# Kernel tuning notes

Hardware: AMD Instinct MI355X
Metric: run time of the kernel (lower is better)

The kernel has to match this reference:

```python
import jax, jax.numpy as jnp
import numpy as np

V, D, NL = 32000, 768, 4
DI, N, DC, DTR = 2 * D, 16, 4, 48  # d_inner, d_state, d_conv, dt_rank
B, L = 2, 1024


def _rmsnorm(x, w, eps=1e-5):
    var = jnp.mean(x * x, axis=-1, keepdims=True)
    return x * jax.lax.rsqrt(var + eps) * w


def _causal_depthwise_conv(x, w, b):
    # x: (B, L, DI), w: (DI, DC), b: (DI,)
    xc = x.transpose(0, 2, 1)  # (B, DI, L)
    out = jax.lax.conv_general_dilated(
        xc, w[:, None, :], window_strides=(1,), padding=[(DC - 1, 0)],
        dimension_numbers=("NCH", "OIH", "NCH"), feature_group_count=DI)
    return (out + b[None, :, None]).transpose(0, 2, 1)


def _selective_scan(u, delta, A, Bm, Cm, Dv):
    # u,delta: (B,L,DI); A: (DI,N); Bm,Cm: (B,L,N); Dv: (DI,)
    dA = jnp.exp(delta[..., None] * A)                       # (B,L,DI,N)
    dBu = delta[..., None] * Bm[:, :, None, :] * u[..., None]  # (B,L,DI,N)

    def step(h, inp):
        dA_t, dBu_t, C_t = inp
        h = dA_t * h + dBu_t                                  # (B,DI,N)
        y = jnp.einsum("bdn,bn->bd", h, C_t)
        return h, y

    h0 = jnp.zeros((u.shape[0], DI, N), u.dtype)
    _, ys = jax.lax.scan(step, h0, (dA.transpose(1, 0, 2, 3),
                                    dBu.transpose(1, 0, 2, 3),
                                    Cm.transpose(1, 0, 2)))
    return ys.transpose(1, 0, 2) + u * Dv


def _mamba_block(x, norm_w, in_w, conv_w, conv_b, xproj_w, dt_w, dt_b,
                 A_log, Dv, out_w):
    xn = _rmsnorm(x, norm_w)
    xz = jnp.einsum("bld,ed->ble", xn, in_w)                 # (B,L,2*DI)
    xb, z = jnp.split(xz, 2, axis=-1)
    xb = jax.nn.silu(_causal_depthwise_conv(xb, conv_w, conv_b))
    x_dbl = jnp.einsum("bld,ed->ble", xb, xproj_w)           # (B,L,DTR+2N)
    dt, Bm, Cm = jnp.split(x_dbl, [DTR, DTR + N], axis=-1)
    delta = jax.nn.softplus(jnp.einsum("blr,dr->bld", dt, dt_w) + dt_b)
    y = _selective_scan(xb, delta, -jnp.exp(A_log), Bm, Cm, Dv)
    y = y * jax.nn.silu(z)
    return x + jnp.einsum("ble,de->bld", y, out_w)


def setup_inputs() -> dict:
    key = jax.random.key(0)
    ks = jax.random.split(key, 16)
    s = lambda k, shape, sc=0.02: jax.random.normal(k, shape, jnp.float32) * sc
    dt_init = jnp.log(jnp.expm1(
        jnp.exp(jax.random.uniform(ks[12], (NL, DI), jnp.float32,
                                   np.log(1e-3), np.log(1e-1)))))
    return {
        "tokens": jax.random.randint(ks[0], (B, L), 0, V),
        "embedding": s(ks[1], (V, D)),
        "W_out_w": s(ks[2], (V, D)),
        "W_out_b": jnp.zeros((V,), jnp.float32),
        "norm_w": jnp.ones((NL, D), jnp.float32),
        "in_proj_w": s(ks[3], (NL, 2 * DI, D)),
        "conv_w": s(ks[4], (NL, DI, DC), 0.1),
        "conv_b": jnp.zeros((NL, DI), jnp.float32),
        "x_proj_w": s(ks[5], (NL, DTR + 2 * N, DI)),
        "dt_proj_w": s(ks[6], (NL, DI, DTR), 0.1),
        "dt_proj_b": dt_init,
        "A_log": jnp.log(jnp.broadcast_to(
            jnp.arange(1, N + 1, dtype=jnp.float32), (NL, DI, N))),
        "D": jnp.ones((NL, DI), jnp.float32),
        "out_proj_w": s(ks[7], (NL, D, DI)),
    }


def reference(tokens, embedding, W_out_w, W_out_b, norm_w, in_proj_w,
              conv_w, conv_b, x_proj_w, dt_proj_w, dt_proj_b, A_log, D,
              out_proj_w):
    x = embedding[tokens]                                    # (B,L,D)
    for i in range(NL):
        x = _mamba_block(x, norm_w[i], in_proj_w[i], conv_w[i], conv_b[i],
                         x_proj_w[i], dt_proj_w[i], dt_proj_b[i],
                         A_log[i], D[i], out_proj_w[i])
    return jnp.einsum("bld,vd->blv", x, W_out_w) + W_out_b
```

## Files before the change

### kernel.cpp

```cpp
#include <hip/hip_runtime.h>
#include <hip/hip_bf16.h>
#include <math.h>

#define BB   2
#define LL   1024
#define DD   768
#define DIN  1536
#define NS   16
#define DCV  4
#define DTRK 48
#define NLAY 4
#define VV   32000
#define ROWS (BB*LL)

#define NCH  32
#define CLEN (LL/NCH)

typedef __attribute__((ext_vector_type(8))) short short8;
typedef __attribute__((ext_vector_type(4))) float f32x4;


__global__ __launch_bounds__(256) void embed_kernel(
    const int* __restrict__ tok, const float* __restrict__ emb,
    float* __restrict__ x) {
  int idx = blockIdx.x * 256 + threadIdx.x;
  int row = idx / DD, c = idx - row * DD;
  x[idx] = emb[(size_t)tok[row] * DD + c];
}

__device__ __forceinline__ void cvt4_bf16(const float* __restrict__ in,
                                          __hip_bfloat16* __restrict__ out,
                                          int i) {
  float4 v = ((const float4*)in)[i];
  __hip_bfloat16 t0 = __float2bfloat16(v.x);
  __hip_bfloat16 t1 = __float2bfloat16(v.y);
  __hip_bfloat16 t2 = __float2bfloat16(v.z);
  __hip_bfloat16 t3 = __float2bfloat16(v.w);
  ushort4 pack = make_ushort4(*(unsigned short*)&t0, *(unsigned short*)&t1,
                              *(unsigned short*)&t2, *(unsigned short*)&t3);
  ((ushort4*)out)[i] = pack;
}

__global__ __launch_bounds__(256) void cvt_bf16_kernel(
    const float* __restrict__ in, __hip_bfloat16* __restrict__ out, int n4) {
  int i = blockIdx.x * 256 + threadIdx.x;
  if (i >= n4) return;
  cvt4_bf16(in, out, i);
}

__global__ __launch_bounds__(256) void cvt3_bf16_kernel(
    const float* __restrict__ i0, __hip_bfloat16* __restrict__ o0, int n0,
    const float* __restrict__ i1, __hip_bfloat16* __restrict__ o1, int n1,
    const float* __restrict__ i2, __hip_bfloat16* __restrict__ o2, int n2) {
  int start = blockIdx.x * 256 + threadIdx.x;
  int stride = gridDim.x * 256;
  for (int j = start; j < n0; j += stride) cvt4_bf16(i0, o0, j);
  for (int j = start; j < n1; j += stride) cvt4_bf16(i1, o1, j);
  for (int j = start; j < n2; j += stride) cvt4_bf16(i2, o2, j);
}

__global__ __launch_bounds__(256) void zero_kernel(float* __restrict__ p,
                                                   int n) {
  int i = blockIdx.x * 256 + threadIdx.x;
  if (i < n) p[i] = 0.0f;
}

__global__ __launch_bounds__(256) void rmsnorm_kernel(
    const float* __restrict__ x, const float* __restrict__ w,
    __hip_bfloat16* __restrict__ xn) {
  int row = blockIdx.x;
  int t = threadIdx.x;
  const float* xr = x + (size_t)row * DD;
  float v0 = xr[t], v1 = xr[t + 256], v2 = xr[t + 512];
  float ss = v0 * v0 + v1 * v1 + v2 * v2;
#pragma unroll
  for (int off = 32; off > 0; off >>= 1) ss += __shfl_down(ss, off);
  __shared__ float sred[4];
  if ((t & 63) == 0) sred[t >> 6] = ss;
  __syncthreads();
  float tot = sred[0] + sred[1] + sred[2] + sred[3];
  float scale = rsqrtf(tot * (1.0f / DD) + 1e-5f);
  __hip_bfloat16* xo = xn + (size_t)row * DD;
  xo[t]       = __float2bfloat16(v0 * scale * w[t]);
  xo[t + 256] = __float2bfloat16(v1 * scale * w[t + 256]);
  xo[t + 512] = __float2bfloat16(v2 * scale * w[t + 512]);
}

__global__ __launch_bounds__(256) void conv_silu_kernel(
    const float* __restrict__ xz, const float* __restrict__ cw,
    const float* __restrict__ cb, float* __restrict__ xb) {
  int idx = blockIdx.x * 256 + threadIdx.x;
  int row = idx / (DIN / 4);
  int d4 = idx - row * (DIN / 4);
  int d = d4 << 2;
  int l = row & (LL - 1);
  const float* col = xz + (size_t)row * (2 * DIN) + d;
  float4 x0 = *(const float4*)col;
  float4 x1 = make_float4(0, 0, 0, 0), x2 = x1, x3 = x1;
  if (l >= 1) x1 = *(const float4*)(col - 2 * DIN);
  if (l >= 2) x2 = *(const float4*)(col - 4 * DIN);
  if (l >= 3) x3 = *(const float4*)(col - 6 * DIN);
  float4 bb = *(const float4*)(cb + d);
  float4 wa = *(const float4*)(cw + (size_t)(d + 0) * 4);
  float4 wb = *(const float4*)(cw + (size_t)(d + 1) * 4);
  float4 wc = *(const float4*)(cw + (size_t)(d + 2) * 4);
  float4 wd = *(const float4*)(cw + (size_t)(d + 3) * 4);
  float4 r;
  r.x = bb.x + wa.w * x0.x + wa.z * x1.x + wa.y * x2.x + wa.x * x3.x;
  r.y = bb.y + wb.w * x0.y + wb.z * x1.y + wb.y * x2.y + wb.x * x3.y;
  r.z = bb.z + wc.w * x0.z + wc.z * x1.z + wc.y * x2.z + wc.x * x3.z;
  r.w = bb.w + wd.w * x0.w + wd.z * x1.w + wd.y * x2.w + wd.x * x3.w;
  r.x = r.x / (1.0f + __expf(-r.x));
  r.y = r.y / (1.0f + __expf(-r.y));
  r.z = r.z / (1.0f + __expf(-r.z));
  r.w = r.w / (1.0f + __expf(-r.w));
  *(float4*)(xb + (size_t)row * DIN + d) = r;
}

__device__ __forceinline__ float softplus_f(float t) {
  return t > 20.0f ? t : log1pf(__expf(t));
}

template <int EPI>
__global__ __launch_bounds__(256) void sgemm_nt(
    const float* __restrict__ A, int lda,
    const float* __restrict__ W, int ldw,
    float* __restrict__ C, int ldc,
    int N, int K, const float* __restrict__ bias) {
  __shared__ float As[16][68];
  __shared__ float Ws[16][68];
  const int tid = threadIdx.x;
  const int tx = tid & 15, ty = tid >> 4;
  const int bm = blockIdx.x, bn = blockIdx.y;
  const int kLen = K / gridDim.z;
  const int kBegin = blockIdx.z * kLen;
  const int kEnd = kBegin + kLen;
  const int lrow = tid >> 2;
  const int lk4 = (tid & 3) << 2;
  const float* Aptr = A + (size_t)(bm * 64 + lrow) * lda + lk4;
  const int wrow = bn * 64 + lrow;
  const float* Wptr = W + (size_t)wrow * ldw + lk4;
  const bool wvalid = wrow < N;
  float c[4][4] = {};
  for (int k0 = kBegin; k0 < kEnd; k0 += 16) {
    float4 a4 = *(const float4*)(Aptr + k0);
    float4 w4 = wvalid ? *(const float4*)(Wptr + k0) : make_float4(0, 0, 0, 0);
    __syncthreads();
    As[lk4 + 0][lrow] = a4.x; As[lk4 + 1][lrow] = a4.y;
    As[lk4 + 2][lrow] = a4.z; As[lk4 + 3][lrow] = a4.w;
    Ws[lk4 + 0][lrow] = w4.x; Ws[lk4 + 1][lrow] = w4.y;
    Ws[lk4 + 2][lrow] = w4.z; Ws[lk4 + 3][lrow] = w4.w;
    __syncthreads();
#pragma unroll
    for (int k = 0; k < 16; k++) {
      float4 a = *(const float4*)&As[k][ty << 2];
      float4 w = *(const float4*)&Ws[k][tx << 2];
      c[0][0] += a.x * w.x; c[0][1] += a.x * w.y; c[0][2] += a.x * w.z; c[0][3] += a.x * w.w;
      c[1][0] += a.y * w.x; c[1][1] += a.y * w.y; c[1][2] += a.y * w.z; c[1][3] += a.y * w.w;
      c[2][0] += a.z * w.x; c[2][1] += a.z * w.y; c[2][2] += a.z * w.z; c[2][3] += a.z * w.w;
      c[3][0] += a.w * w.x; c[3][1] += a.w * w.y; c[3][2] += a.w * w.z; c[3][3] += a.w * w.w;
    }
  }
  const int m0 = bm * 64 + (ty << 2);
  const int n0 = bn * 64 + (tx << 2);
  const bool split = gridDim.z > 1;
#pragma unroll
  for (int i = 0; i < 4; i++) {
    float* crow = C + (size_t)(m0 + i) * ldc;
#pragma unroll
    for (int j = 0; j < 4; j++) {
      int n = n0 + j;
      if (n < N) {
        float v = c[i][j];
        if constexpr (EPI == 1) v = softplus_f(v + bias[n]);
        if (split) atomicAdd(&crow[n], v);
        else crow[n] = v;
      }
    }
  }
}


__device__ __forceinline__ void gload16(const void* g, void* l) {
  __builtin_amdgcn_global_load_lds(
      (const __attribute__((address_space(1))) void*)g,
      (__attribute__((address_space(3))) void*)l, 16, 0, 0);
}

template <int EPI>
__global__ __launch_bounds__(256) void bgemm_nt(
    const __hip_bfloat16* __restrict__ A, int lda,
    const __hip_bfloat16* __restrict__ W, int ldw,
    float* __restrict__ C, int ldc,
    int K, const float* __restrict__ bias) {
  __shared__ short As[2][128 * 32];
  __shared__ short Ws[2][128 * 32];
  const int tid = threadIdx.x;
  const int wave = tid >> 6, lane = tid & 63;
  const int wm = wave >> 1, wn = wave & 1;

  const int nbx = gridDim.x;
  const int nwg = nbx * gridDim.y;
  int flat = blockIdx.y * nbx + blockIdx.x;
  if ((nwg & 7) == 0) {
    int chunk = nwg >> 3;
    flat = (flat & 7) * chunk + (flat >> 3);
  }
  const int tileM = (flat % nbx) * 128, tileN = (flat / nbx) * 128;

  const short* Ag = (const short*)A;
  const short* Wg = (const short*)W;
  const int cid0 = tid, cid1 = tid + 256;
  const size_t aOff0 = (size_t)(tileM + (cid0 >> 2)) * lda + (cid0 & 3) * 8;
  const size_t aOff1 = (size_t)(tileM + (cid1 >> 2)) * lda + (cid1 & 3) * 8;
  const size_t wOff0 = (size_t)(tileN + (cid0 >> 2)) * ldw + (cid0 & 3) * 8;
  const size_t wOff1 = (size_t)(tileN + (cid1 >> 2)) * ldw + (cid1 & 3) * 8;
  const int wb0 = wave * 512, wb1 = 2048 + wave * 512;

  const int fr = lane & 15, fq = lane >> 4;
  f32x4 acc[4][4] = {};

  for (int k0 = 0; k0 < K; k0 += 64) {
    gload16(Ag + aOff0 + k0, As[0] + wb0);
    gload16(Ag + aOff1 + k0, As[0] + wb1);
    gload16(Wg + wOff0 + k0, Ws[0] + wb0);
    gload16(Wg + wOff1 + k0, Ws[0] + wb1);
    gload16(Ag + aOff0 + k0 + 32, As[1] + wb0);
    gload16(Ag + aOff1 + k0 + 32, As[1] + wb1);
    gload16(Wg + wOff0 + k0 + 32, Ws[1] + wb0);
    gload16(Wg + wOff1 + k0 + 32, Ws[1] + wb1);
    __syncthreads();
#pragma unroll
    for (int s = 0; s < 2; s++) {
      short8 afr[4], bfr[4];
#pragma unroll
      for (int t = 0; t < 4; t++) {
        afr[t] = *(const short8*)(As[s] + (wm * 64 + t * 16 + fr) * 32 + fq * 8);
        bfr[t] = *(const short8*)(Ws[s] + (wn * 64 + t * 16 + fr) * 32 + fq * 8);
      }
#pragma unroll
      for (int mt = 0; mt < 4; mt++)
#pragma unroll
        for (int nt = 0; nt < 4; nt++)
          acc[mt][nt] = __builtin_amdgcn_mfma_f32_16x16x32_bf16(
              afr[mt], bfr[nt], acc[mt][nt], 0, 0, 0);
    }
    __syncthreads();
  }

#pragma unroll
  for (int mt = 0; mt < 4; mt++) {
#pragma unroll
    for (int r = 0; r < 4; r++) {
      int row = tileM + wm * 64 + mt * 16 + fq * 4 + r;
      float* crow = C + (size_t)row * ldc;
#pragma unroll
      for (int nt = 0; nt < 4; nt++) {
        int col = tileN + wn * 64 + nt * 16 + fr;
        float v = acc[mt][nt][r];
        if constexpr (EPI == 2) v += crow[col];
        else if constexpr (EPI == 3) v += bias[col];
        crow[col] = v;
      }
    }
  }
}


__global__ __launch_bounds__(256) void scan_pass1(
    const float* __restrict__ u,
    const float* __restrict__ dlt,
    const float* __restrict__ xdbl,
    const float* __restrict__ A_log,
    float* __restrict__ qbuf,
    float* __restrict__ sdel) {
  const int d = blockIdx.x * 256 + threadIdx.x;
  const int c = blockIdx.y;
  const int b = blockIdx.z;
  float Ac2[NS];
  {
    const float* ar = A_log + (size_t)d * NS;
#pragma unroll
    for (int j = 0; j < NS; j++) Ac2[j] = -__expf(ar[j]) * 1.44269504f;
  }
  const int l0 = c * CLEN;
  const float* ur = u   + ((size_t)b * LL + l0) * DIN + d;
  const float* dr = dlt + ((size_t)b * LL + l0) * DIN + d;
  const float* br = xdbl + ((size_t)b * LL + l0) * 80 + DTRK;
  float h[NS];
#pragma unroll
  for (int j = 0; j < NS; j++) h[j] = 0.0f;
  float sd = 0.0f;
  for (int t = 0; t < CLEN; t++) {
    float dl = dr[(size_t)t * DIN];
    float ul = ur[(size_t)t * DIN];
    float Bv[NS];
    *(float4*)&Bv[0]  = *(const float4*)(br + (size_t)t * 80);
    *(float4*)&Bv[4]  = *(const float4*)(br + (size_t)t * 80 + 4);
    *(float4*)&Bv[8]  = *(const float4*)(br + (size_t)t * 80 + 8);
    *(float4*)&Bv[12] = *(const float4*)(br + (size_t)t * 80 + 12);
    sd += dl;
    float du = dl * ul;
#pragma unroll
    for (int j = 0; j < NS; j++)
      h[j] = exp2f(dl * Ac2[j]) * h[j] + du * Bv[j];
  }
  float* qo = qbuf + (((size_t)b * NCH + c) * DIN + d) * NS;
#pragma unroll
  for (int j = 0; j < NS; j += 4)
    *(float4*)(qo + j) = make_float4(h[j], h[j + 1], h[j + 2], h[j + 3]);
  sdel[((size_t)b * NCH + c) * DIN + d] = sd;
}

__global__ __launch_bounds__(256) void scan_pass2(
    const float* __restrict__ qbuf, const float* __restrict__ sdel,
    const float* __restrict__ A_log, float* __restrict__ hstart) {
  const int e = blockIdx.x * 256 + threadIdx.x;
  const int n = e & (NS - 1);
  const int d = e >> 4;
  const int b = blockIdx.y;
  float Ac2 = -__expf(A_log[(size_t)d * NS + n]) * 1.44269504f;
  float h = 0.0f;
  for (int c = 0; c < NCH; c++) {
    hstart[(((size_t)b * NCH + c) * DIN + d) * NS + n] = h;
    if (c + 1 < NCH) {
      float sd = sdel[((size_t)b * NCH + c) * DIN + d];
      float q  = qbuf[(((size_t)b * NCH + c) * DIN + d) * NS + n];
      h = exp2f(Ac2 * sd) * h + q;
    }
  }
}

__global__ __launch_bounds__(256) void scan_pass3(
    const float* __restrict__ u,
    const float* __restrict__ dlt,
    const float* __restrict__ xdbl,
    const float* __restrict__ xz,
    const float* __restrict__ A_log,
    const float* __restrict__ Dv,
    const float* __restrict__ hstart,
    __hip_bfloat16* __restrict__ y) {
  const int d = blockIdx.x * 256 + threadIdx.x;
  const int c = blockIdx.y;
  const int b = blockIdx.z;
  float Ac2[NS];
  {
    const float* ar = A_log + (size_t)d * NS;
#pragma unroll
    for (int j = 0; j < NS; j++) Ac2[j] = -__expf(ar[j]) * 1.44269504f;
  }
  const float Dd = Dv[d];
  float h[NS];
  {
    const float* hs = hstart + (((size_t)b * NCH + c) * DIN + d) * NS;
#pragma unroll
    for (int j = 0; j < NS; j += 4) {
      float4 hv = *(const float4*)(hs + j);
      h[j] = hv.x; h[j + 1] = hv.y; h[j + 2] = hv.z; h[j + 3] = hv.w;
    }
  }
  const int l0 = c * CLEN;
  const float* ur = u   + ((size_t)b * LL + l0) * DIN + d;
  const float* dr = dlt + ((size_t)b * LL + l0) * DIN + d;
  const float* br = xdbl + ((size_t)b * LL + l0) * 80 + DTRK;
  const float* cr = br + NS;
  const float* zr = xz + ((size_t)b * LL + l0) * (2 * DIN) + DIN + d;
  __hip_bfloat16* yr = y + ((size_t)b * LL + l0) * DIN + d;
  for (int t = 0; t < CLEN; t++) {
    float dl = dr[(size_t)t * DIN];
    float ul = ur[(size_t)t * DIN];
    float zl = zr[(size_t)t * (2 * DIN)];
    float Bv[NS], Cv[NS];
    *(float4*)&Bv[0]  = *(const float4*)(br + (size_t)t * 80);
    *(float4*)&Bv[4]  = *(const float4*)(br + (size_t)t * 80 + 4);
    *(float4*)&Bv[8]  = *(const float4*)(br + (size_t)t * 80 + 8);
    *(float4*)&Bv[12] = *(const float4*)(br + (size_t)t * 80 + 12);
    *(float4*)&Cv[0]  = *(const float4*)(cr + (size_t)t * 80);
    *(float4*)&Cv[4]  = *(const float4*)(cr + (size_t)t * 80 + 4);
    *(float4*)&Cv[8]  = *(const float4*)(cr + (size_t)t * 80 + 8);
    *(float4*)&Cv[12] = *(const float4*)(cr + (size_t)t * 80 + 12);
    float du = dl * ul;
    float acc = 0.0f;
#pragma unroll
    for (int j = 0; j < NS; j++) {
      h[j] = exp2f(dl * Ac2[j]) * h[j] + du * Bv[j];
      acc += h[j] * Cv[j];
    }
    acc += ul * Dd;
    float sig = 1.0f / (1.0f + __expf(-zl));
    yr[(size_t)t * DIN] = __float2bfloat16(acc * (zl * sig));
  }
}


extern "C" void kernel_launch(void* const* d_in, const int* in_sizes, int n_in,
                              void* d_out, int out_size, void* d_ws,
                              size_t ws_size, hipStream_t stream) {
  const int*   tokens    = (const int*)d_in[0];
  const float* embedding = (const float*)d_in[1];
  const float* W_out_w   = (const float*)d_in[2];
  const float* W_out_b   = (const float*)d_in[3];
  const float* norm_w    = (const float*)d_in[4];
  const float* in_proj_w = (const float*)d_in[5];
  const float* conv_w    = (const float*)d_in[6];
  const float* conv_b    = (const float*)d_in[7];
  const float* x_proj_w  = (const float*)d_in[8];
  const float* dt_proj_w = (const float*)d_in[9];
  const float* dt_proj_b = (const float*)d_in[10];
  const float* A_log     = (const float*)d_in[11];
  const float* Dvec      = (const float*)d_in[12];
  const float* out_proj_w= (const float*)d_in[13];
  float* out = (float*)d_out;

  float* ws = (float*)d_ws;
  float* x    = ws;
  float* xz   = x + (size_t)ROWS * DD;
  float* xb   = xz + (size_t)ROWS * 2 * DIN;
  float* xdbl = xb + (size_t)ROWS * DIN;
  float* dlt  = xdbl + (size_t)ROWS * 80;
  __hip_bfloat16* bfbase = (__hip_bfloat16*)(dlt + (size_t)ROWS * DIN);
  __hip_bfloat16* xnb  = bfbase;
  __hip_bfloat16* ybb  = xnb + (size_t)ROWS * DD;
  __hip_bfloat16* xbf  = ybb + (size_t)ROWS * DIN;
  __hip_bfloat16* wInB = xbf + (size_t)ROWS * DD;
  __hip_bfloat16* wOpB = wInB + (size_t)NLAY * 2 * DIN * DD;
  __hip_bfloat16* wLgB = wOpB + (size_t)NLAY * DD * DIN;
  float* qbuf   = (float*)(wLgB + (size_t)VV * DD);
  float* sdel   = qbuf + (size_t)BB * NCH * DIN * NS;
  float* hstart = sdel + (size_t)BB * NCH * DIN;

  cvt3_bf16_kernel<<<2048, 256, 0, stream>>>(
      in_proj_w, wInB, NLAY * 2 * DIN * DD / 4,
      out_proj_w, wOpB, NLAY * DD * DIN / 4,
      W_out_w, wLgB, VV * DD / 4);

  embed_kernel<<<ROWS * DD / 256, 256, 0, stream>>>(tokens, embedding, x);

  for (int i = 0; i < NLAY; i++) {
    rmsnorm_kernel<<<ROWS, 256, 0, stream>>>(x, norm_w + (size_t)i * DD, xnb);
    bgemm_nt<0><<<dim3(16, 24), 256, 0, stream>>>(
        xnb, DD, wInB + (size_t)i * 2 * DIN * DD, DD, xz, 2 * DIN, DD,
        nullptr);
    conv_silu_kernel<<<ROWS * DIN / 4 / 256, 256, 0, stream>>>(
        xz, conv_w + (size_t)i * DIN * DCV, conv_b + (size_t)i * DIN, xb);
    zero_kernel<<<ROWS * 80 / 256, 256, 0, stream>>>(xdbl, ROWS * 80);
    sgemm_nt<0><<<dim3(32, 2, 8), 256, 0, stream>>>(
        xb, DIN, x_proj_w + (size_t)i * (DTRK + 2 * NS) * DIN, DIN, xdbl,
        DTRK + 2 * NS, DTRK + 2 * NS, DIN, nullptr);
    sgemm_nt<1><<<dim3(32, 24), 256, 0, stream>>>(
        xdbl, DTRK + 2 * NS, dt_proj_w + (size_t)i * DIN * DTRK, DTRK, dlt,
        DIN, DIN, DTRK, dt_proj_b + (size_t)i * DIN);
    const float* Ai = A_log + (size_t)i * DIN * NS;
    scan_pass1<<<dim3(DIN / 256, NCH - 1, BB), 256, 0, stream>>>(
        xb, dlt, xdbl, Ai, qbuf, sdel);
    scan_pass2<<<dim3(DIN * NS / 256, BB), 256, 0, stream>>>(
        qbuf, sdel, Ai, hstart);
    scan_pass3<<<dim3(DIN / 256, NCH, BB), 256, 0, stream>>>(
        xb, dlt, xdbl, xz, Ai, Dvec + (size_t)i * DIN, hstart, ybb);
    bgemm_nt<2><<<dim3(16, 6), 256, 0, stream>>>(
        ybb, DIN, wOpB + (size_t)i * DD * DIN, DIN, x, DD, DIN, nullptr);
  }

  {
    int n4 = ROWS * DD / 4;
    cvt_bf16_kernel<<<(n4 + 255) / 256, 256, 0, stream>>>(x, xbf, n4);
  }
  bgemm_nt<3><<<dim3(16, 250), 256, 0, stream>>>(
      xbf, DD, wLgB, DD, out, VV, DD, W_out_b);
}
```

Measured before the change: 1.349 ms.

## Shrink bf16 GEMM N-tile to 64 and add split-K for out_proj

The bf16 MFMA GEMM now uses 128x64 output tiles instead of 128x128, which doubles the grid for the in_proj and logits GEMMs. It also gains a split-K path over gridDim.z whose partial results are accumulated into C with atomicAdd. The out_proj GEMM uses that path (K split in two, 384 blocks) to fill more CUs, and the xdbl zeroing kernel is replaced by hipMemsetAsync. The aim is more parallelism on the small GEMMs; the costs are lower data reuse per tile, more memory traffic on the large logits GEMM, and non-deterministic float atomics.

```diff
diff --git a/kernel.cpp b/kernel.cpp
--- a/kernel.cpp
+++ b/kernel.cpp
@@ -57,12 +57,6 @@
   for (int j = start; j < n0; j += stride) cvt4_bf16(i0, o0, j);
   for (int j = start; j < n1; j += stride) cvt4_bf16(i1, o1, j);
   for (int j = start; j < n2; j += stride) cvt4_bf16(i2, o2, j);
-}
-
-__global__ __launch_bounds__(256) void zero_kernel(float* __restrict__ p,
-                                                   int n) {
-  int i = blockIdx.x * 256 + threadIdx.x;
-  if (i < n) p[i] = 0.0f;
 }
 
 __global__ __launch_bounds__(256) void rmsnorm_kernel(
@@ -194,7 +188,7 @@
     float* __restrict__ C, int ldc,
     int K, const float* __restrict__ bias) {
   __shared__ short As[2][128 * 32];
-  __shared__ short Ws[2][128 * 32];
+  __shared__ short Ws[2][64 * 32];
   const int tid = threadIdx.x;
   const int wave = tid >> 6, lane = tid & 63;
   const int wm = wave >> 1, wn = wave & 1;
@@ -206,7 +200,10 @@
     int chunk = nwg >> 3;
     flat = (flat & 7) * chunk + (flat >> 3);
   }
-  const int tileM = (flat % nbx) * 128, tileN = (flat / nbx) * 128;
+  const int tileM = (flat % nbx) * 128, tileN = (flat / nbx) * 64;
+
+  const int kLen = K / gridDim.z;
+  const int kBegin = blockIdx.z * kLen, kEnd = kBegin + kLen;
 
   const short* Ag = (const short*)A;
   const short* Wg = (const short*)W;
@@ -214,40 +211,39 @@
   const size_t aOff0 = (size_t)(tileM + (cid0 >> 2)) * lda + (cid0 & 3) * 8;
   const size_t aOff1 = (size_t)(tileM + (cid1 >> 2)) * lda + (cid1 & 3) * 8;
   const size_t wOff0 = (size_t)(tileN + (cid0 >> 2)) * ldw + (cid0 & 3) * 8;
-  const size_t wOff1 = (size_t)(tileN + (cid1 >> 2)) * ldw + (cid1 & 3) * 8;
-  const int wb0 = wave * 512, wb1 = 2048 + wave * 512;
+  const int wb = wave * 512;
 
   const int fr = lane & 15, fq = lane >> 4;
-  f32x4 acc[4][4] = {};
-
-  for (int k0 = 0; k0 < K; k0 += 64) {
-    gload16(Ag + aOff0 + k0, As[0] + wb0);
-    gload16(Ag + aOff1 + k0, As[0] + wb1);
-    gload16(Wg + wOff0 + k0, Ws[0] + wb0);
-    gload16(Wg + wOff1 + k0, Ws[0] + wb1);
-    gload16(Ag + aOff0 + k0 + 32, As[1] + wb0);
-    gload16(Ag + aOff1 + k0 + 32, As[1] + wb1);
-    gload16(Wg + wOff0 + k0 + 32, Ws[1] + wb0);
-    gload16(Wg + wOff1 + k0 + 32, Ws[1] + wb1);
+  f32x4 acc[4][2] = {};
+
+  for (int k0 = kBegin; k0 < kEnd; k0 += 64) {
+#pragma unroll
+    for (int s = 0; s < 2; s++) {
+      gload16(Ag + aOff0 + k0 + s * 32, As[s] + wb);
+      gload16(Ag + aOff1 + k0 + s * 32, As[s] + 2048 + wb);
+      gload16(Wg + wOff0 + k0 + s * 32, Ws[s] + wb);
+    }
     __syncthreads();
 #pragma unroll
     for (int s = 0; s < 2; s++) {
-      short8 afr[4], bfr[4];
-#pragma unroll
-      for (int t = 0; t < 4; t++) {
+      short8 afr[4], bfr[2];
+#pragma unroll
+      for (int t = 0; t < 4; t++)
         afr[t] = *(const short8*)(As[s] + (wm * 64 + t * 16 + fr) * 32 + fq * 8);
-        bfr[t] = *(const short8*)(Ws[s] + (wn * 64 + t * 16 + fr) * 32 + fq * 8);
-      }
+#pragma unroll
+      for (int t = 0; t < 2; t++)
+        bfr[t] = *(const short8*)(Ws[s] + (wn * 32 + t * 16 + fr) * 32 + fq * 8);
 #pragma unroll
       for (int mt = 0; mt < 4; mt++)
 #pragma unroll
-        for (int nt = 0; nt < 4; nt++)
+        for (int nt = 0; nt < 2; nt++)
           acc[mt][nt] = __builtin_amdgcn_mfma_f32_16x16x32_bf16(
               afr[mt], bfr[nt], acc[mt][nt], 0, 0, 0);
     }
     __syncthreads();
   }
 
+  const bool split = gridDim.z > 1;
 #pragma unroll
   for (int mt = 0; mt < 4; mt++) {
 #pragma unroll
@@ -255,12 +251,16 @@
       int row = tileM + wm * 64 + mt * 16 + fq * 4 + r;
       float* crow = C + (size_t)row * ldc;
 #pragma unroll
-      for (int nt = 0; nt < 4; nt++) {
-        int col = tileN + wn * 64 + nt * 16 + fr;
+      for (int nt = 0; nt < 2; nt++) {
+        int col = tileN + wn * 32 + nt * 16 + fr;
         float v = acc[mt][nt][r];
-        if constexpr (EPI == 2) v += crow[col];
-        else if constexpr (EPI == 3) v += bias[col];
-        crow[col] = v;
+        if (split) {
+          atomicAdd(&crow[col], v);
+        } else {
+          if constexpr (EPI == 2) v += crow[col];
+          else if constexpr (EPI == 3) v += bias[col];
+          crow[col] = v;
+        }
       }
     }
   }
@@ -438,12 +438,12 @@
 
   for (int i = 0; i < NLAY; i++) {
     rmsnorm_kernel<<<ROWS, 256, 0, stream>>>(x, norm_w + (size_t)i * DD, xnb);
-    bgemm_nt<0><<<dim3(16, 24), 256, 0, stream>>>(
+    bgemm_nt<0><<<dim3(16, 48), 256, 0, stream>>>(
         xnb, DD, wInB + (size_t)i * 2 * DIN * DD, DD, xz, 2 * DIN, DD,
         nullptr);
     conv_silu_kernel<<<ROWS * DIN / 4 / 256, 256, 0, stream>>>(
         xz, conv_w + (size_t)i * DIN * DCV, conv_b + (size_t)i * DIN, xb);
-    zero_kernel<<<ROWS * 80 / 256, 256, 0, stream>>>(xdbl, ROWS * 80);
+    hipMemsetAsync(xdbl, 0, (size_t)ROWS * 80 * sizeof(float), stream);
     sgemm_nt<0><<<dim3(32, 2, 8), 256, 0, stream>>>(
         xb, DIN, x_proj_w + (size_t)i * (DTRK + 2 * NS) * DIN, DIN, xdbl,
         DTRK + 2 * NS, DTRK + 2 * NS, DIN, nullptr);
@@ -457,7 +457,7 @@
         qbuf, sdel, Ai, hstart);
     scan_pass3<<<dim3(DIN / 256, NCH, BB), 256, 0, stream>>>(
         xb, dlt, xdbl, xz, Ai, Dvec + (size_t)i * DIN, hstart, ybb);
-    bgemm_nt<2><<<dim3(16, 6), 256, 0, stream>>>(
+    bgemm_nt<2><<<dim3(16, 12, 2), 256, 0, stream>>>(
         ybb, DIN, wOpB + (size_t)i * DD * DIN, DIN, x, DD, DIN, nullptr);
   }
 
@@ -465,6 +465,6 @@
     int n4 = ROWS * DD / 4;
     cvt_bf16_kernel<<<(n4 + 255) / 256, 256, 0, stream>>>(x, xbf, n4);
   }
-  bgemm_nt<3><<<dim3(16, 250), 256, 0, stream>>>(
+  bgemm_nt<3><<<dim3(16, 500), 256, 0, stream>>>(
       xbf, DD, wLgB, DD, out, VV, DD, W_out_b);
 }
```

Measured after the change: 1.363 ms. Within noise of the previous version (+1.0%).
